# Kernel optimization log

Hardware: AMD Instinct MI355X
Metric: run time of the kernel (lower is better)

## Reference

```python
import jax, jax.numpy as jnp
import numpy as np

EPS = 1e-5

def conv3x3(x, W, b):
    # NCHW 3x3 conv, padding=1 (SAME)
    y = jax.lax.conv_general_dilated(x, W, (1, 1), ((1, 1), (1, 1)),
                                     dimension_numbers=('NCHW', 'OIHW', 'NCHW'))
    return y + b[None, :, None, None]

def bn_relu(x, gamma, beta):
    # BatchNorm2d in training mode: batch statistics over (N,H,W)
    m = x.mean(axis=(0, 2, 3), keepdims=True)
    v = x.var(axis=(0, 2, 3), keepdims=True)
    xn = (x - m) * jax.lax.rsqrt(v + EPS)
    return jax.nn.relu(xn * gamma[None, :, None, None] + beta[None, :, None, None])

def haar_dwt2(x):
    # pywt.dwt2(x, 'db1') for even H,W: cA=LL, cH=row-detail/col-approx,
    # cV=row-approx/col-detail, cD=HH; each 0.5*(+-a +-b +-c +-d)
    a = x[:, :, 0::2, 0::2]
    b = x[:, :, 0::2, 1::2]
    c = x[:, :, 1::2, 0::2]
    d = x[:, :, 1::2, 1::2]
    cA = (a + b + c + d) * 0.5
    cH = (a + b - c - d) * 0.5
    cV = (a - b + c - d) * 0.5
    cD = (a - b - c + d) * 0.5
    return jnp.concatenate([cA, cH, cV, cD], axis=1)  # [B, 4C, H/2, W/2]

def setup_inputs() -> dict:
    key = jax.random.key(0)
    ks = jax.random.split(key, 4)
    B, Cin, Cout, H, W = 8, 64, 128, 256, 256
    inputs = jax.random.normal(ks[0], (B, Cin, H, W), dtype=jnp.float32)
    W1 = jax.random.normal(ks[1], (Cout, Cin, 3, 3), dtype=jnp.float32) * 0.05
    W2 = jax.random.normal(ks[2], (Cout, Cout, 3, 3), dtype=jnp.float32) * 0.05
    W3 = jax.random.normal(ks[3], (Cout, 4 * Cout, 3, 3), dtype=jnp.float32) * 0.05
    z = jnp.zeros((Cout,), jnp.float32)
    o = jnp.ones((Cout,), jnp.float32)
    return {"inputs": inputs,
            "W1": W1, "b1": z, "g1": o, "be1": z,
            "W2": W2, "b2": z, "g2": o, "be2": z,
            "W3": W3, "b3": z, "g3": o, "be3": z}

def reference(inputs, W1, b1, g1, be1, W2, b2, g2, be2, W3, b3, g3, be3):
    h = bn_relu(conv3x3(inputs, W1, b1), g1, be1)
    skip_con = bn_relu(conv3x3(h, W2, b2), g2, be2)          # [B, out_c, H, W]
    # original detaches before the pywt round-trip
    dwt = haar_dwt2(jax.lax.stop_gradient(skip_con))          # [B, 4*out_c, H/2, W/2]
    dwt_out = bn_relu(conv3x3(dwt, W3, b3), g3, be3)          # [B, out_c, H/2, W/2]
    return (skip_con, dwt_out)
```

## Files before the change

kernel.cpp:

```cpp
#include <hip/hip_runtime.h>

typedef __attribute__((ext_vector_type(8))) short bf16x8;
typedef __attribute__((ext_vector_type(4))) short bf16x4;
typedef __attribute__((ext_vector_type(4))) float f32x4;

__device__ __forceinline__ float bf2f(ushort u) {
  union { unsigned int i; float f; } v; v.i = ((unsigned int)u) << 16; return v.f;
}
__device__ __forceinline__ ushort f2bf(float f) {
  union { float f; unsigned int i; } v; v.f = f;
  unsigned int x = v.i;
  unsigned int r = (x + 0x7fffu + ((x >> 16) & 1u)) >> 16;
  return (ushort)r;
}

__global__ void zero_f32(float* p, int n) {
  int i = blockIdx.x * 256 + threadIdx.x;
  if (i < n) p[i] = 0.f;
}

__global__ void pack_w(const float* __restrict__ W, ushort* __restrict__ Wp, int Cin) {
  int ncic = Cin >> 5;
  int total = 9 * ncic * 8 * 64 * 8;
  for (int idx = blockIdx.x * 256 + threadIdx.x; idx < total; idx += gridDim.x * 256) {
    int j = idx & 7;
    int l = (idx >> 3) & 63;
    int cf = (idx >> 9) & 7;
    int rest = idx >> 12;
    int cic = rest % ncic;
    int tap = rest / ncic;
    int co = cf * 16 + (l & 15);
    int ci = cic * 32 + ((l >> 4) * 8) + j;
    int ky = tap / 3, kx = tap % 3;
    Wp[idx] = f2bf(W[((co * Cin + ci) * 3 + ky) * 3 + kx]);
  }
}

__global__ __launch_bounds__(256)
void nchw2nhwc(const float* __restrict__ in, ushort* __restrict__ out) {
  const int n  = blockIdx.y;
  const int p0 = blockIdx.x << 6;
  const int tid = threadIdx.x;
  __shared__ ushort t[64 * 72];
  {
    int c  = tid >> 2;
    int pq = (tid & 3) << 4;
    const float* ip = in + (((size_t)(n * 64 + c)) << 16) + p0 + pq;
#pragma unroll
    for (int k = 0; k < 4; ++k) {
      float4 f = *(const float4*)(ip + k * 4);
      int p = pq + k * 4;
      t[(p + 0) * 72 + c] = f2bf(f.x);
      t[(p + 1) * 72 + c] = f2bf(f.y);
      t[(p + 2) * 72 + c] = f2bf(f.z);
      t[(p + 3) * 72 + c] = f2bf(f.w);
    }
  }
  __syncthreads();
#pragma unroll
  for (int k = 0; k < 2; ++k) {
    int id = k * 256 + tid;
    int cj = id & 7, p = id >> 3;
    bf16x8 v = *(const bf16x8*)&t[p * 72 + cj * 8];
    *(bf16x8*)(out + ((((size_t)n << 16) + p0 + p) << 6) + cj * 8) = v;
  }
}

__device__ __forceinline__ bf16x8 bnrelu8(bf16x8 v, const float* __restrict__ coef, int c0) {
  float4 a0 = *(const float4*)(coef + c0);
  float4 a1 = *(const float4*)(coef + c0 + 4);
  float4 b0 = *(const float4*)(coef + 128 + c0);
  float4 b1 = *(const float4*)(coef + 128 + c0 + 4);
  bf16x8 r;
  r[0] = (short)f2bf(fmaxf(a0.x * bf2f((ushort)v[0]) + b0.x, 0.f));
  r[1] = (short)f2bf(fmaxf(a0.y * bf2f((ushort)v[1]) + b0.y, 0.f));
  r[2] = (short)f2bf(fmaxf(a0.z * bf2f((ushort)v[2]) + b0.z, 0.f));
  r[3] = (short)f2bf(fmaxf(a0.w * bf2f((ushort)v[3]) + b0.w, 0.f));
  r[4] = (short)f2bf(fmaxf(a1.x * bf2f((ushort)v[4]) + b1.x, 0.f));
  r[5] = (short)f2bf(fmaxf(a1.y * bf2f((ushort)v[5]) + b1.y, 0.f));
  r[6] = (short)f2bf(fmaxf(a1.z * bf2f((ushort)v[6]) + b1.z, 0.f));
  r[7] = (short)f2bf(fmaxf(a1.w * bf2f((ushort)v[7]) + b1.w, 0.f));
  return r;
}

template<int MODE>
__global__ __launch_bounds__(256)
void conv_mfma(const ushort* __restrict__ src, const ushort* __restrict__ Wp,
               const float* __restrict__ bias, const float* __restrict__ coef,
               ushort* __restrict__ out, float* __restrict__ sSum, float* __restrict__ sSsq,
               int Cin, int H, int W)
{
  const int ncic = Cin >> 5;
  const int x0 = blockIdx.x << 6;
  const int y0 = blockIdx.y << 1;
  const int n  = blockIdx.z;
  const int tid = threadIdx.x;
  const int wv = tid >> 6, l = tid & 63, l15 = l & 15, l4 = l >> 4;

  __shared__ __align__(16) char smem[17408];
  ushort* lds = (ushort*)smem;
  ushort* eps = (ushort*)smem;

  f32x4 acc[2][2][4];
#pragma unroll
  for (int yr = 0; yr < 2; ++yr)
#pragma unroll
    for (int f = 0; f < 2; ++f)
#pragma unroll
      for (int xf = 0; xf < 4; ++xf) acc[yr][f][xf] = (f32x4){0.f, 0.f, 0.f, 0.f};

  const size_t HW = (size_t)H * W;
  const ushort* srcn = src + (size_t)n * HW * Cin;
  const int cjc = (tid & 3) << 3;

  int off[5], wch[5];
#pragma unroll
  for (int it = 0; it < 5; ++it) {
    int i = it * 256 + tid;
    int cj = i & 3, p = i >> 2;
    int row = p / 66, xt = p - row * 66;
    int ry = y0 + row - 1, gx = x0 + xt - 1;
    bool ok = (i < 1056) && ((unsigned)ry < (unsigned)H) && ((unsigned)gx < (unsigned)W);
    off[it] = ok ? (int)((ry * W + gx) * Cin + (cj << 3)) : -1;
    wch[it] = ((row << 2) | cj) * 66 + xt;
  }

  for (int cic = 0; cic < ncic; ++cic) {
    __syncthreads();
#pragma unroll
    for (int it = 0; it < 5; ++it) {
      if (it < 4 || tid < 32) {
        bf16x8 v = {};
        if (off[it] >= 0) {
          v = *(const bf16x8*)(srcn + off[it] + (cic << 5));
          if (MODE == 1) v = bnrelu8(v, coef, (cic << 5) + cjc);
        }
        *(bf16x8*)&lds[wch[it] << 3] = v;
      }
    }
    __syncthreads();

    const ushort* wp = Wp + (((size_t)cic * 8) + (wv << 1)) * 512 + ((size_t)l << 3);
    const size_t tstride = (size_t)ncic * 4096;

#pragma unroll
    for (int tap = 0; tap < 9; ++tap) {
      const int ky = tap / 3, kx = tap % 3;
      bf16x8 afr[2];
#pragma unroll
      for (int f = 0; f < 2; ++f)
        afr[f] = *(const bf16x8*)(wp + (size_t)tap * tstride + (f << 9));
      bf16x8 bfr[2][4];
#pragma unroll
      for (int yr = 0; yr < 2; ++yr)
#pragma unroll
        for (int xf = 0; xf < 4; ++xf) {
          int row = yr + ky;
          int xt = (xf << 4) + l15 + kx;
          bfr[yr][xf] = *(const bf16x8*)&lds[(((row << 2) | l4) * 66 + xt) << 3];
        }
#pragma unroll
      for (int f = 0; f < 2; ++f)
#pragma unroll
        for (int yr = 0; yr < 2; ++yr)
#pragma unroll
          for (int xf = 0; xf < 4; ++xf)
            acc[yr][f][xf] = __builtin_amdgcn_mfma_f32_16x16x32_bf16(afr[f], bfr[yr][xf], acc[yr][f][xf], 0, 0, 0);
    }
  }

  float sm[2][4] = {{0.f}}, sq[2][4] = {{0.f}};
  const int cb = (wv << 5) + (l4 << 2);
  for (int yr = 0; yr < 2; ++yr) {
    __syncthreads();
#pragma unroll
    for (int f = 0; f < 2; ++f) {
      const int cf = cb + (f << 4);
      float4 bv = *(const float4*)(bias + cf);
#pragma unroll
      for (int xf = 0; xf < 4; ++xf) {
        float v0 = acc[yr][f][xf][0] + bv.x;
        float v1 = acc[yr][f][xf][1] + bv.y;
        float v2 = acc[yr][f][xf][2] + bv.z;
        float v3 = acc[yr][f][xf][3] + bv.w;
        sm[f][0] += v0; sq[f][0] += v0 * v0;
        sm[f][1] += v1; sq[f][1] += v1 * v1;
        sm[f][2] += v2; sq[f][2] += v2 * v2;
        sm[f][3] += v3; sq[f][3] += v3 * v3;
        bf16x4 u;
        u[0] = (short)f2bf(v0); u[1] = (short)f2bf(v1);
        u[2] = (short)f2bf(v2); u[3] = (short)f2bf(v3);
        *(bf16x4*)&eps[((xf << 4) + l15) * 136 + cf] = u;
      }
    }
    __syncthreads();
    {
      const int xx = tid >> 2, c0 = (tid & 3) << 5;
      ushort* op = out + ((size_t)n * HW + (size_t)(y0 + yr) * W + x0 + xx) * 128 + c0;
#pragma unroll
      for (int k = 0; k < 4; ++k)
        *(bf16x8*)(op + (k << 3)) = *(const bf16x8*)&eps[xx * 136 + c0 + (k << 3)];
    }
  }

  const int rep = (int)((blockIdx.z * gridDim.y + blockIdx.y) * gridDim.x + blockIdx.x) & 31;
#pragma unroll
  for (int f = 0; f < 2; ++f)
#pragma unroll
    for (int j = 0; j < 4; ++j) {
      float s = sm[f][j], q = sq[f][j];
#pragma unroll
      for (int o = 1; o < 16; o <<= 1) { s += __shfl_xor(s, o); q += __shfl_xor(q, o); }
      if (l15 == 0) {
        int co = cb + (f << 4) + j;
        atomicAdd(&sSum[rep * 128 + co], s);
        atomicAdd(&sSsq[rep * 128 + co], q);
      }
    }
}

__global__ void bn_finalize(const float* __restrict__ sSum, const float* __restrict__ sSsq,
                            const float* __restrict__ g, const float* __restrict__ be,
                            float* __restrict__ coef, float invN)
{
  int c = threadIdx.x;
  float S = 0.f, Q = 0.f;
  for (int r = 0; r < 32; ++r) { S += sSum[r * 128 + c]; Q += sSsq[r * 128 + c]; }
  float m = S * invN;
  float v = Q * invN - m * m;
  float a = g[c] / sqrtf(v + 1e-5f);
  coef[c] = a;
  coef[128 + c] = be[c] - m * a;
}

__global__ __launch_bounds__(256)
void skip_dwt2(const ushort* __restrict__ skipRaw, const float* __restrict__ coef,
               float* __restrict__ outSkip, ushort* __restrict__ dwt)
{
  const int x0 = blockIdx.x << 6;
  const int oy = blockIdx.y;
  const int n  = blockIdx.z >> 2;
  const int ct = blockIdx.z & 3;
  const int y0 = oy << 1;
  const int tid = threadIdx.x;
  __shared__ float t32[32 * 2 * 68];

#pragma unroll
  for (int it = 0; it < 2; ++it) {
    int i = it * 256 + tid;
    int cj = i & 3, x = (i >> 2) & 63, r = i >> 8;
    int c0 = (ct << 5) + (cj << 3);
    bf16x8 v = *(const bf16x8*)(skipRaw + (((size_t)n << 16) + (size_t)(y0 + r) * 256 + x0 + x) * 128 + c0);
    float4 a0 = *(const float4*)(coef + c0);
    float4 a1 = *(const float4*)(coef + c0 + 4);
    float4 b0 = *(const float4*)(coef + 128 + c0);
    float4 b1 = *(const float4*)(coef + 128 + c0 + 4);
    float av[8] = {a0.x, a0.y, a0.z, a0.w, a1.x, a1.y, a1.z, a1.w};
    float bv[8] = {b0.x, b0.y, b0.z, b0.w, b1.x, b1.y, b1.z, b1.w};
    int cl = cj << 3;
#pragma unroll
    for (int k = 0; k < 8; ++k)
      t32[((cl + k) * 2 + r) * 68 + x] = fmaxf(av[k] * bf2f((ushort)v[k]) + bv[k], 0.f);
  }
  __syncthreads();

  {
    int c = tid >> 3, x8 = (tid & 7) << 3;
    float* op = outSkip + (((size_t)(n * 128 + (ct << 5) + c)) << 16) + (size_t)y0 * 256 + x0 + x8;
#pragma unroll
    for (int r = 0; r < 2; ++r) {
      float4 r0 = *(const float4*)&t32[(c * 2 + r) * 68 + x8];
      float4 r1 = *(const float4*)&t32[(c * 2 + r) * 68 + x8 + 4];
      *(float4*)(op + (size_t)r * 256) = r0;
      *(float4*)(op + (size_t)r * 256 + 4) = r1;
    }
  }

  if (tid < 128) {
    int cj = tid & 3, ox = tid >> 2;
    int cl = cj << 3;
    bf16x8 oA, oH, oV, oD;
#pragma unroll
    for (int k = 0; k < 8; ++k) {
      int c = cl + k;
      float p00 = t32[(c * 2 + 0) * 68 + 2 * ox];
      float p01 = t32[(c * 2 + 0) * 68 + 2 * ox + 1];
      float p10 = t32[(c * 2 + 1) * 68 + 2 * ox];
      float p11 = t32[(c * 2 + 1) * 68 + 2 * ox + 1];
      oA[k] = (short)f2bf((p00 + p01 + p10 + p11) * 0.5f);
      oH[k] = (short)f2bf((p00 + p01 - p10 - p11) * 0.5f);
      oV[k] = (short)f2bf((p00 - p01 + p10 - p11) * 0.5f);
      oD[k] = (short)f2bf((p00 - p01 - p10 + p11) * 0.5f);
    }
    size_t db = ((size_t)n * 16384 + (size_t)oy * 128 + (x0 >> 1) + ox) * 512 + (ct << 5) + cl;
    *(bf16x8*)(dwt + db)       = oA;
    *(bf16x8*)(dwt + db + 128) = oH;
    *(bf16x8*)(dwt + db + 256) = oV;
    *(bf16x8*)(dwt + db + 384) = oD;
  }
}

__global__ __launch_bounds__(256)
void bn_transpose_out(const ushort* __restrict__ src, const float* __restrict__ coef,
                      float* __restrict__ dst, int H, int W)
{
  const int n  = blockIdx.z >> 2;
  const int cc = blockIdx.z & 3;
  const int x0 = blockIdx.x << 6;
  const int y  = blockIdx.y;
  const int tid = threadIdx.x;
  __shared__ float t[32 * 68];
  const size_t HW = (size_t)H * W;
  {
    int p = tid >> 2, cj = tid & 3;
    int c0 = (cc << 5) + (cj << 3);
    bf16x8 v = *(const bf16x8*)(src + ((size_t)n * HW + (size_t)y * W + x0 + p) * 128 + c0);
    float4 a0 = *(const float4*)(coef + c0);
    float4 a1 = *(const float4*)(coef + c0 + 4);
    float4 b0 = *(const float4*)(coef + 128 + c0);
    float4 b1 = *(const float4*)(coef + 128 + c0 + 4);
    int cl = cj << 3;
    t[(cl + 0) * 68 + p] = fmaxf(a0.x * bf2f((ushort)v[0]) + b0.x, 0.f);
    t[(cl + 1) * 68 + p] = fmaxf(a0.y * bf2f((ushort)v[1]) + b0.y, 0.f);
    t[(cl + 2) * 68 + p] = fmaxf(a0.z * bf2f((ushort)v[2]) + b0.z, 0.f);
    t[(cl + 3) * 68 + p] = fmaxf(a0.w * bf2f((ushort)v[3]) + b0.w, 0.f);
    t[(cl + 4) * 68 + p] = fmaxf(a1.x * bf2f((ushort)v[4]) + b1.x, 0.f);
    t[(cl + 5) * 68 + p] = fmaxf(a1.y * bf2f((ushort)v[5]) + b1.y, 0.f);
    t[(cl + 6) * 68 + p] = fmaxf(a1.z * bf2f((ushort)v[6]) + b1.z, 0.f);
    t[(cl + 7) * 68 + p] = fmaxf(a1.w * bf2f((ushort)v[7]) + b1.w, 0.f);
  }
  __syncthreads();
  {
    int c = tid >> 3, x8 = (tid & 7) << 3;
    float4 r0 = *(const float4*)&t[c * 68 + x8];
    float4 r1 = *(const float4*)&t[c * 68 + x8 + 4];
    float* op = dst + ((size_t)(n * 128 + (cc << 5) + c)) * HW + (size_t)y * W + x0 + x8;
    *(float4*)op = r0;
    *(float4*)(op + 4) = r1;
  }
}

extern "C" void kernel_launch(void* const* d_in, const int* in_sizes, int n_in,
                              void* d_out, int out_size, void* d_ws, size_t ws_size,
                              hipStream_t stream)
{
  const float* input = (const float*)d_in[0];
  const float* W1  = (const float*)d_in[1];
  const float* b1  = (const float*)d_in[2];
  const float* g1  = (const float*)d_in[3];
  const float* be1 = (const float*)d_in[4];
  const float* W2  = (const float*)d_in[5];
  const float* b2  = (const float*)d_in[6];
  const float* g2  = (const float*)d_in[7];
  const float* be2 = (const float*)d_in[8];
  const float* W3  = (const float*)d_in[9];
  const float* b3  = (const float*)d_in[10];
  const float* g3  = (const float*)d_in[11];
  const float* be3 = (const float*)d_in[12];

  char* ws = (char*)d_ws;
  ushort* h_raw    = (ushort*)(ws + 0);
  ushort* skip_raw = (ushort*)(ws + 134217728);
  ushort* dwt      = (ushort*)(ws + 268435456);
  ushort* in_nhwc  = (ushort*)(ws + 268435456);
  ushort* raw3     = (ushort*)(ws + 402653184);
  float*  stats    = (float*)(ws + 436207616);
  float*  s1 = stats,          *q1 = stats + 4096;
  float*  s2 = stats + 8192,   *q2 = stats + 12288;
  float*  s3 = stats + 16384,  *q3 = stats + 20480;
  float*  coef = (float*)(ws + 436305920);
  float*  c1 = coef, *c2 = coef + 256, *c3 = coef + 512;
  ushort* Wp1 = (ushort*)(ws + 436308992);
  ushort* Wp2 = (ushort*)(ws + 436456448);
  ushort* Wp3 = (ushort*)(ws + 436751360);

  zero_f32<<<96, 256, 0, stream>>>(stats, 24576);
  pack_w<<<288, 256, 0, stream>>>(W1, Wp1, 64);
  pack_w<<<576, 256, 0, stream>>>(W2, Wp2, 128);
  pack_w<<<2304, 256, 0, stream>>>(W3, Wp3, 512);
  nchw2nhwc<<<dim3(1024, 8), 256, 0, stream>>>(input, in_nhwc);

  conv_mfma<0><<<dim3(4, 128, 8), 256, 0, stream>>>(in_nhwc, Wp1, b1, nullptr,
                                                    h_raw, s1, q1, 64, 256, 256);
  bn_finalize<<<1, 128, 0, stream>>>(s1, q1, g1, be1, c1, 1.f / 524288.f);

  conv_mfma<1><<<dim3(4, 128, 8), 256, 0, stream>>>(h_raw, Wp2, b2, c1,
                                                    skip_raw, s2, q2, 128, 256, 256);
  bn_finalize<<<1, 128, 0, stream>>>(s2, q2, g2, be2, c2, 1.f / 524288.f);

  skip_dwt2<<<dim3(4, 128, 32), 256, 0, stream>>>(skip_raw, c2, (float*)d_out, dwt);

  conv_mfma<0><<<dim3(2, 64, 8), 256, 0, stream>>>(dwt, Wp3, b3, nullptr,
                                                   raw3, s3, q3, 512, 128, 128);
  bn_finalize<<<1, 128, 0, stream>>>(s3, q3, g3, be3, c3, 1.f / 131072.f);

  bn_transpose_out<<<dim3(2, 128, 32), 256, 0, stream>>>(raw3, c3, (float*)d_out + 67108864, 128, 128);
}
```

Before: 765.0 us.

## Double-buffer conv input tiles with direct global-to-LDS loads

Splits the conv kernel in two. Convs 1 and 3 use a new kernel that loads input tiles straight into LDS with global_load_lds and double-buffers them, so the next channel chunk streams in while MFMAs run on the current one. Conv 2 keeps a register-staged path because it applies BN+ReLU while loading. The DMA path changes the LDS tile layout to pixel-major with the channel group innermost, zero-fills the tile once for border blocks, and doubles LDS use, which may lower occupancy and adds bank-conflict risk.

```diff
diff --git a/kernel.cpp b/kernel.cpp
--- a/kernel.cpp
+++ b/kernel.cpp
@@ -12,6 +12,11 @@
   unsigned int x = v.i;
   unsigned int r = (x + 0x7fffu + ((x >> 16) & 1u)) >> 16;
   return (ushort)r;
+}
+
+__device__ __forceinline__ void gload_lds16(const ushort* g, ushort* l) {
+  __builtin_amdgcn_global_load_lds((const __attribute__((address_space(1))) void*)g,
+                                   (__attribute__((address_space(3))) void*)l, 16, 0, 0);
 }
 
 __global__ void zero_f32(float* p, int n) {
@@ -85,10 +90,10 @@
 
 template<int MODE>
 __global__ __launch_bounds__(256)
-void conv_mfma(const ushort* __restrict__ src, const ushort* __restrict__ Wp,
-               const float* __restrict__ bias, const float* __restrict__ coef,
-               ushort* __restrict__ out, float* __restrict__ sSum, float* __restrict__ sSsq,
-               int Cin, int H, int W)
+void conv_reg(const ushort* __restrict__ src, const ushort* __restrict__ Wp,
+              const float* __restrict__ bias, const float* __restrict__ coef,
+              ushort* __restrict__ out, float* __restrict__ sSum, float* __restrict__ sSsq,
+              int Cin, int H, int W)
 {
   const int ncic = Cin >> 5;
   const int x0 = blockIdx.x << 6;
@@ -110,10 +115,123 @@
       for (int xf = 0; xf < 4; ++xf) acc[yr][f][xf] = (f32x4){0.f, 0.f, 0.f, 0.f};
 
   const size_t HW = (size_t)H * W;
+
+  for (int cic = 0; cic < ncic; ++cic) {
+    __syncthreads();
+    for (int i = tid; i < 1056; i += 256) {
+      int cj = i & 3;
+      int t = i >> 2;
+      int row = t / 66;
+      int xt = t - row * 66;
+      int ry = y0 + row - 1;
+      int gx = x0 + xt - 1;
+      bf16x8 v = {};
+      if ((unsigned)ry < (unsigned)H && (unsigned)gx < (unsigned)W) {
+        const ushort* p = src + ((size_t)n * HW + (size_t)ry * W + gx) * Cin + (cic << 5) + (cj << 3);
+        v = *(const bf16x8*)p;
+        if (MODE == 1) v = bnrelu8(v, coef, (cic << 5) + (cj << 3));
+      }
+      *(bf16x8*)&lds[(((row << 2) | cj) * 66 + xt) << 3] = v;
+    }
+    __syncthreads();
+
+#pragma unroll
+    for (int tap = 0; tap < 9; ++tap) {
+      const int ky = tap / 3, kx = tap % 3;
+      bf16x8 afr[2];
+#pragma unroll
+      for (int f = 0; f < 2; ++f) {
+        const int cf = (wv << 1) | f;
+        afr[f] = *(const bf16x8*)(Wp + (((size_t)(tap * ncic + cic) * 8 + cf) * 64 + l) * 8);
+      }
+      bf16x8 bfr[2][4];
+#pragma unroll
+      for (int yr = 0; yr < 2; ++yr)
+#pragma unroll
+        for (int xf = 0; xf < 4; ++xf) {
+          int row = yr + ky;
+          int xt = (xf << 4) + l15 + kx;
+          bfr[yr][xf] = *(const bf16x8*)&lds[(((row << 2) | l4) * 66 + xt) << 3];
+        }
+#pragma unroll
+      for (int f = 0; f < 2; ++f)
+#pragma unroll
+        for (int yr = 0; yr < 2; ++yr)
+#pragma unroll
+          for (int xf = 0; xf < 4; ++xf)
+            acc[yr][f][xf] = __builtin_amdgcn_mfma_f32_16x16x32_bf16(afr[f], bfr[yr][xf], acc[yr][f][xf], 0, 0, 0);
+    }
+  }
+
+  float sm[2][4] = {{0.f}}, sq[2][4] = {{0.f}};
+  const int cb = (wv << 5) + (l4 << 2);
+  for (int yr = 0; yr < 2; ++yr) {
+    __syncthreads();
+#pragma unroll
+    for (int f = 0; f < 2; ++f) {
+      const int cf = cb + (f << 4);
+      float4 bv = *(const float4*)(bias + cf);
+#pragma unroll
+      for (int xf = 0; xf < 4; ++xf) {
+        float v0 = acc[yr][f][xf][0] + bv.x;
+        float v1 = acc[yr][f][xf][1] + bv.y;
+        float v2 = acc[yr][f][xf][2] + bv.z;
+        float v3 = acc[yr][f][xf][3] + bv.w;
+        sm[f][0] += v0; sq[f][0] += v0 * v0;
+        sm[f][1] += v1; sq[f][1] += v1 * v1;
+        sm[f][2] += v2; sq[f][2] += v2 * v2;
+        sm[f][3] += v3; sq[f][3] += v3 * v3;
+        bf16x4 u;
+        u[0] = (short)f2bf(v0); u[1] = (short)f2bf(v1);
+        u[2] = (short)f2bf(v2); u[3] = (short)f2bf(v3);
+        *(bf16x4*)&eps[((xf << 4) + l15) * 136 + cf] = u;
+      }
+    }
+    __syncthreads();
+    {
+      const int xx = tid >> 2, c0 = (tid & 3) << 5;
+      ushort* op = out + ((size_t)n * HW + (size_t)(y0 + yr) * W + x0 + xx) * 128 + c0;
+#pragma unroll
+      for (int k = 0; k < 4; ++k)
+        *(bf16x8*)(op + (k << 3)) = *(const bf16x8*)&eps[xx * 136 + c0 + (k << 3)];
+    }
+  }
+
+  const int rep = (int)((blockIdx.z * gridDim.y + blockIdx.y) * gridDim.x + blockIdx.x) & 31;
+#pragma unroll
+  for (int f = 0; f < 2; ++f)
+#pragma unroll
+    for (int j = 0; j < 4; ++j) {
+      float s = sm[f][j], q = sq[f][j];
+#pragma unroll
+      for (int o = 1; o < 16; o <<= 1) { s += __shfl_xor(s, o); q += __shfl_xor(q, o); }
+      if (l15 == 0) {
+        int co = cb + (f << 4) + j;
+        atomicAdd(&sSum[rep * 128 + co], s);
+        atomicAdd(&sSsq[rep * 128 + co], q);
+      }
+    }
+}
+
+__global__ __launch_bounds__(256)
+void conv_dma(const ushort* __restrict__ src, const ushort* __restrict__ Wp,
+              const float* __restrict__ bias,
+              ushort* __restrict__ out, float* __restrict__ sSum, float* __restrict__ sSsq,
+              int Cin, int H, int W)
+{
+  const int ncic = Cin >> 5;
+  const int x0 = blockIdx.x << 6;
+  const int y0 = blockIdx.y << 1;
+  const int n  = blockIdx.z;
+  const int tid = threadIdx.x;
+  const int wv = tid >> 6, l = tid & 63, l15 = l & 15, l4 = l >> 4;
+
+  __shared__ __align__(16) ushort smem[2 * 8448];
+
+  const size_t HW = (size_t)H * W;
   const ushort* srcn = src + (size_t)n * HW * Cin;
-  const int cjc = (tid & 3) << 3;
-
-  int off[5], wch[5];
+
+  int off[5];
 #pragma unroll
   for (int it = 0; it < 5; ++it) {
     int i = it * 256 + tid;
@@ -122,34 +240,41 @@
     int ry = y0 + row - 1, gx = x0 + xt - 1;
     bool ok = (i < 1056) && ((unsigned)ry < (unsigned)H) && ((unsigned)gx < (unsigned)W);
     off[it] = ok ? (int)((ry * W + gx) * Cin + (cj << 3)) : -1;
-    wch[it] = ((row << 2) | cj) * 66 + xt;
-  }
-
-  for (int cic = 0; cic < ncic; ++cic) {
-    __syncthreads();
+  }
+
+  if (x0 == 0 || x0 + 64 >= W || y0 == 0 || y0 + 2 >= H) {
+    for (int k = tid; k < 2112; k += 256) *(bf16x8*)&smem[k << 3] = (bf16x8){};
+  }
+  __syncthreads();
+
+  f32x4 acc[2][2][4];
+#pragma unroll
+  for (int yr = 0; yr < 2; ++yr)
+#pragma unroll
+    for (int f = 0; f < 2; ++f)
+#pragma unroll
+      for (int xf = 0; xf < 4; ++xf) acc[yr][f][xf] = (f32x4){0.f, 0.f, 0.f, 0.f};
+
+  auto STAGE = [&](ushort* buf, int cic) {
+    const int coff = cic << 5;
 #pragma unroll
     for (int it = 0; it < 5; ++it) {
-      if (it < 4 || tid < 32) {
-        bf16x8 v = {};
-        if (off[it] >= 0) {
-          v = *(const bf16x8*)(srcn + off[it] + (cic << 5));
-          if (MODE == 1) v = bnrelu8(v, coef, (cic << 5) + cjc);
-        }
-        *(bf16x8*)&lds[wch[it] << 3] = v;
-      }
-    }
-    __syncthreads();
-
-    const ushort* wp = Wp + (((size_t)cic * 8) + (wv << 1)) * 512 + ((size_t)l << 3);
-    const size_t tstride = (size_t)ncic * 4096;
-
+      ushort* ldst = buf + ((it < 4 ? (it * 256 + (wv << 6)) : 1024) << 3);
+      if (off[it] >= 0)
+        gload_lds16(srcn + off[it] + coff, ldst);
+    }
+  };
+
+  auto COMPUTE = [&](const ushort* buf, int cic) {
 #pragma unroll
     for (int tap = 0; tap < 9; ++tap) {
       const int ky = tap / 3, kx = tap % 3;
       bf16x8 afr[2];
 #pragma unroll
-      for (int f = 0; f < 2; ++f)
-        afr[f] = *(const bf16x8*)(wp + (size_t)tap * tstride + (f << 9));
+      for (int f = 0; f < 2; ++f) {
+        const int cf = (wv << 1) | f;
+        afr[f] = *(const bf16x8*)(Wp + (((size_t)(tap * ncic + cic) * 8 + cf) * 64 + l) * 8);
+      }
       bf16x8 bfr[2][4];
 #pragma unroll
       for (int yr = 0; yr < 2; ++yr)
@@ -157,7 +282,7 @@
         for (int xf = 0; xf < 4; ++xf) {
           int row = yr + ky;
           int xt = (xf << 4) + l15 + kx;
-          bfr[yr][xf] = *(const bf16x8*)&lds[(((row << 2) | l4) * 66 + xt) << 3];
+          bfr[yr][xf] = *(const bf16x8*)&buf[((((row * 66 + xt) << 2) | l4)) << 3];
         }
 #pragma unroll
       for (int f = 0; f < 2; ++f)
@@ -167,9 +292,21 @@
           for (int xf = 0; xf < 4; ++xf)
             acc[yr][f][xf] = __builtin_amdgcn_mfma_f32_16x16x32_bf16(afr[f], bfr[yr][xf], acc[yr][f][xf], 0, 0, 0);
     }
+  };
+
+  STAGE(smem, 0);
+  __syncthreads();
+
+  int cur = 0;
+  for (int cic = 0; cic < ncic; ++cic) {
+    if (cic + 1 < ncic) STAGE(smem + (cur ^ 1) * 8448, cic + 1);
+    COMPUTE(smem + cur * 8448, cic);
+    __syncthreads();
+    cur ^= 1;
   }
 
   float sm[2][4] = {{0.f}}, sq[2][4] = {{0.f}};
+  ushort* eps = smem;
   const int cb = (wv << 5) + (l4 << 2);
   for (int yr = 0; yr < 2; ++yr) {
     __syncthreads();
@@ -380,18 +517,18 @@
   pack_w<<<2304, 256, 0, stream>>>(W3, Wp3, 512);
   nchw2nhwc<<<dim3(1024, 8), 256, 0, stream>>>(input, in_nhwc);
 
-  conv_mfma<0><<<dim3(4, 128, 8), 256, 0, stream>>>(in_nhwc, Wp1, b1, nullptr,
-                                                    h_raw, s1, q1, 64, 256, 256);
+  conv_dma<<<dim3(4, 128, 8), 256, 0, stream>>>(in_nhwc, Wp1, b1,
+                                                h_raw, s1, q1, 64, 256, 256);
   bn_finalize<<<1, 128, 0, stream>>>(s1, q1, g1, be1, c1, 1.f / 524288.f);
 
-  conv_mfma<1><<<dim3(4, 128, 8), 256, 0, stream>>>(h_raw, Wp2, b2, c1,
-                                                    skip_raw, s2, q2, 128, 256, 256);
+  conv_reg<1><<<dim3(4, 128, 8), 256, 0, stream>>>(h_raw, Wp2, b2, c1,
+                                                   skip_raw, s2, q2, 128, 256, 256);
   bn_finalize<<<1, 128, 0, stream>>>(s2, q2, g2, be2, c2, 1.f / 524288.f);
 
   skip_dwt2<<<dim3(4, 128, 32), 256, 0, stream>>>(skip_raw, c2, (float*)d_out, dwt);
 
-  conv_mfma<0><<<dim3(2, 64, 8), 256, 0, stream>>>(dwt, Wp3, b3, nullptr,
-                                                   raw3, s3, q3, 512, 128, 128);
+  conv_dma<<<dim3(2, 64, 8), 256, 0, stream>>>(dwt, Wp3, b3,
+                                               raw3, s3, q3, 512, 128, 128);
   bn_finalize<<<1, 128, 0, stream>>>(s3, q3, g3, be3, c3, 1.f / 131072.f);
 
   bn_transpose_out<<<dim3(2, 128, 32), 256, 0, stream>>>(raw3, c3, (float*)d_out + 67108864, 128, 128);
```

Measured after the change: 696.3 us (median of 2 runs). 9.0% less time.
